# Performance work log

Hardware: AMD Instinct MI355X
Metric: run time of the kernel (lower is better)

Reference implementation:

```python
import jax, jax.numpy as jnp
import numpy as np

S = 2048       # seq_len
D = 1024       # d_model
H = 16         # heads
DK = 64        # d_k = d_v = D // H


def setup_inputs() -> dict:
    key = jax.random.key(0)
    ks = jax.random.split(key, 12)
    sc_in = 1.0 / np.sqrt(D)
    return {
        "Q": jax.random.normal(ks[0], (S, D), jnp.float32),
        "K": jax.random.normal(ks[1], (S, D), jnp.float32),
        "V": jax.random.normal(ks[2], (S, D), jnp.float32),
        # stacked per-head projection weights (torch Linear math: x @ W + b, W stored [in,out])
        "Wq": jax.random.normal(ks[3], (H, D, DK), jnp.float32) * sc_in,
        "bq": jnp.zeros((H, DK), jnp.float32),
        "Wk": jax.random.normal(ks[4], (H, D, DK), jnp.float32) * sc_in,
        "bk": jnp.zeros((H, DK), jnp.float32),
        "Wv": jax.random.normal(ks[5], (H, D, DK), jnp.float32) * sc_in,
        "bv": jnp.zeros((H, DK), jnp.float32),
        "Wo": jax.random.normal(ks[6], (H * DK, D), jnp.float32) * (1.0 / np.sqrt(H * DK)),
        "bo": jnp.zeros((D,), jnp.float32),
    }


def reference(Q, K, V, Wq, bq, Wk, bk, Wv, bv, Wo, bo):
    # per-head projections, all heads at once: [S,D] x [H,D,DK] -> [H,S,DK]
    q = jnp.einsum("sd,hdk->hsk", Q, Wq) + bq[:, None, :]
    k = jnp.einsum("sd,hdk->hsk", K, Wk) + bk[:, None, :]
    v = jnp.einsum("sd,hdk->hsk", V, Wv) + bv[:, None, :]
    # scaled dot-product attention per head: [H,S,S]
    scores = jnp.einsum("hsk,htk->hst", q, k) / jnp.sqrt(jnp.asarray(DK, q.dtype))
    attn = jax.nn.softmax(scores, axis=-1)
    heads = jnp.einsum("hst,htv->hsv", attn, v)          # [H,S,DK]
    concat = heads.transpose(1, 0, 2).reshape(S, H * DK)  # [S, H*DK]
    return concat @ Wo + bo                               # [S, D]
```

## Files before the change

kernel.cpp:

```cpp
#include <hip/hip_runtime.h>
#include <stdint.h>

#define S_LEN 2048
#define D_MODEL 1024
#define NH 16
#define DKV 64

typedef unsigned short u16;
typedef __bf16 bf16x8 __attribute__((ext_vector_type(8)));
typedef float f32x4 __attribute__((ext_vector_type(4)));

__device__ __forceinline__ u16 f2bf(float f) {
  union { float f; uint32_t u; } v; v.f = f;
  uint32_t r = v.u + 0x7FFFu + ((v.u >> 16) & 1u);
  return (u16)(r >> 16);
}
__device__ __forceinline__ uint32_t pkbf(float lo, float hi) {
  union { float f; uint32_t u; } a, b; a.f = lo; b.f = hi;
  return ((b.u + 0x8000u) & 0xFFFF0000u) | ((a.u + 0x8000u) >> 16);
}
__device__ __forceinline__ void gl16(const u16* g, u16* l) {
  __builtin_amdgcn_global_load_lds(
      (const __attribute__((address_space(1))) unsigned int*)g,
      (__attribute__((address_space(3))) unsigned int*)l, 16, 0, 0);
}

__global__ __launch_bounds__(256) void conv_qkv_k(
    const float* __restrict__ Q, const float* __restrict__ K,
    const float* __restrict__ V, u16* __restrict__ out) {
  const float* src = (blockIdx.z == 0) ? Q : (blockIdx.z == 1) ? K : V;
  u16* dst = out + (size_t)blockIdx.z * S_LEN * D_MODEL;
  size_t i = ((size_t)blockIdx.x * blockDim.x + threadIdx.x) * 4;
  const float4 v = *(const float4*)(src + i);
  union { u16 h[4]; uint2 u2; } o;
  o.h[0] = f2bf(v.x); o.h[1] = f2bf(v.y); o.h[2] = f2bf(v.z); o.h[3] = f2bf(v.w);
  *(uint2*)(dst + i) = o.u2;
}

__global__ __launch_bounds__(256) void transpose_qkvw_k(
    const float* __restrict__ Wq, const float* __restrict__ Wk,
    const float* __restrict__ Wv, u16* __restrict__ Wqt,
    u16* __restrict__ Wkt, u16* __restrict__ Wvt) {
  __shared__ float tile[32][33];
  const int which = blockIdx.z >> 4, head = blockIdx.z & 15;
  const float* ip = ((which == 0) ? Wq : (which == 1) ? Wk : Wv) + (size_t)head * D_MODEL * DKV;
  u16* op = ((which == 0) ? Wqt : (which == 1) ? Wkt : Wvt) + (size_t)head * D_MODEL * DKV;
  int r0 = blockIdx.y * 32, c0 = blockIdx.x * 32;
  int tr = threadIdx.x >> 5, tc = threadIdx.x & 31;
#pragma unroll
  for (int i = 0; i < 4; i++)
    tile[tr + i * 8][tc] = ip[(size_t)(r0 + tr + i * 8) * DKV + c0 + tc];
  __syncthreads();
#pragma unroll
  for (int i = 0; i < 4; i++) {
    int c = tr + i * 8;
    op[(size_t)(c0 + c) * D_MODEL + r0 + tc] = f2bf(tile[tc][c]);
  }
}

__global__ __launch_bounds__(256) void transpose_conv_k(
    const float* __restrict__ in, u16* __restrict__ out, int R, int C) {
  __shared__ float tile[32][33];
  int r0 = blockIdx.y * 32, c0 = blockIdx.x * 32;
  int tr = threadIdx.x >> 5, tc = threadIdx.x & 31;
#pragma unroll
  for (int i = 0; i < 4; i++)
    tile[tr + i * 8][tc] = in[(size_t)(r0 + tr + i * 8) * C + c0 + tc];
  __syncthreads();
#pragma unroll
  for (int i = 0; i < 4; i++) {
    int c = tr + i * 8;
    out[(size_t)(c0 + c) * R + r0 + tc] = f2bf(tile[tc][c]);
  }
}

__global__ __launch_bounds__(256, 2) void proj_gemm_k(
    const u16* __restrict__ qkvb, const u16* __restrict__ Wqt,
    const u16* __restrict__ Wkt, const u16* __restrict__ Wvt,
    const float* __restrict__ bq, const float* __restrict__ bk,
    const float* __restrict__ bv,
    u16* __restrict__ qb, u16* __restrict__ kb, u16* __restrict__ vT) {
  const int z = blockIdx.z;
  const int m0 = blockIdx.x * 128, n0 = blockIdx.y * 128;
  const u16* A = qkvb + (size_t)z * S_LEN * D_MODEL;
  const u16* Bt = (z == 0) ? Wqt : (z == 1) ? Wkt : Wvt;
  const float* bias = (z == 0) ? bq : (z == 1) ? bk : bv;
  const float scale = (z == 0) ? 0.18033688f : 1.0f;

  __shared__ __align__(16) u16 smem[4 * 8192];
  const int tid = threadIdx.x;
  const int w = tid >> 6, lane = tid & 63, quad = lane >> 4, l15 = lane & 15;
  const int wm = (w >> 1) * 64, wn = (w & 1) * 64;
  const int pb = w * 256;

  f32x4 acc[4][4] = {};

  {
    u16* As = smem; u16* Bs = smem + 16384;
#pragma unroll
    for (int e = 0; e < 4; e++) {
      int p = pb + e * 64 + lane;
      int r = p >> 3, cg = (p & 7) ^ (r & 7);
      gl16(&A[(size_t)(m0 + r) * D_MODEL + cg * 8], As + (pb + e * 64) * 8);
      gl16(&Bt[(size_t)(n0 + r) * D_MODEL + cg * 8], Bs + (pb + e * 64) * 8);
    }
  }
  for (int it = 0; it < 16; it++) {
    __syncthreads();
    if (it < 15) {
      const int k0 = (it + 1) * 64;
      u16* As = smem + ((it + 1) & 1) * 8192;
      u16* Bs = smem + 16384 + ((it + 1) & 1) * 8192;
#pragma unroll
      for (int e = 0; e < 4; e++) {
        int p = pb + e * 64 + lane;
        int r = p >> 3, cg = (p & 7) ^ (r & 7);
        gl16(&A[(size_t)(m0 + r) * D_MODEL + k0 + cg * 8], As + (pb + e * 64) * 8);
        gl16(&Bt[(size_t)(n0 + r) * D_MODEL + k0 + cg * 8], Bs + (pb + e * 64) * 8);
      }
    }
    const u16* As = smem + (it & 1) * 8192;
    const u16* Bs = smem + 16384 + (it & 1) * 8192;
#pragma unroll
    for (int kc = 0; kc < 2; kc++) {
      bf16x8 af[4], bfr[4];
      const int c = kc * 4 + quad;
#pragma unroll
      for (int t = 0; t < 4; t++) {
        int ma = wm + t * 16 + l15, na = wn + t * 16 + l15;
        af[t] = *(const bf16x8*)&As[(ma * 8 + (c ^ (ma & 7))) * 8];
        bfr[t] = *(const bf16x8*)&Bs[(na * 8 + (c ^ (na & 7))) * 8];
      }
#pragma unroll
      for (int tm = 0; tm < 4; tm++)
#pragma unroll
        for (int tn = 0; tn < 4; tn++)
          acc[tm][tn] = __builtin_amdgcn_mfma_f32_16x16x32_bf16(af[tm], bfr[tn], acc[tm][tn], 0, 0, 0);
    }
  }

  if (z < 2) {
    u16* O = (z == 0) ? qb : kb;
#pragma unroll
    for (int tm = 0; tm < 4; tm++)
#pragma unroll
      for (int tn = 0; tn < 4; tn++)
#pragma unroll
        for (int r = 0; r < 4; r++) {
          int row = m0 + wm + tm * 16 + quad * 4 + r;
          int col = n0 + wn + tn * 16 + l15;
          O[(size_t)row * D_MODEL + col] = f2bf((acc[tm][tn][r] + bias[col]) * scale);
        }
  } else {
#pragma unroll
    for (int tm = 0; tm < 4; tm++)
#pragma unroll
      for (int tn = 0; tn < 4; tn++) {
        int col = n0 + wn + tn * 16 + l15;
        int row0 = m0 + wm + tm * 16 + quad * 4;
        float b = bias[col];
        union { u16 h[4]; uint2 u2; } o;
#pragma unroll
        for (int r = 0; r < 4; r++) o.h[r] = f2bf(acc[tm][tn][r] + b);
        *(uint2*)&vT[(size_t)col * S_LEN + row0] = o.u2;
      }
  }
}

__global__ __launch_bounds__(512) void attn_k(
    const u16* __restrict__ qb, const u16* __restrict__ kb,
    const u16* __restrict__ vT, u16* __restrict__ conc) {
  const int h = blockIdx.y, qblk = blockIdx.x * 64;
  const int tid = threadIdx.x;
  const int w = tid >> 6, lane = tid & 63, quad = lane >> 4, l15 = lane & 15;
  const int half = w >> 2, wq = w & 3;
  const int q0 = qblk + wq * 16;

  __shared__ __align__(16) u16 smem[25600];
  u16* Kh = smem + half * 4096;
  u16* Vh = smem + 8192 + half * 4096;
  u16* Pw = smem + 16384 + w * 1152;

  bf16x8 qf[2];
#pragma unroll
  for (int kc = 0; kc < 2; kc++)
    qf[kc] = *(const bf16x8*)&qb[(size_t)(q0 + l15) * D_MODEL + h * 64 + kc * 32 + quad * 8];

  const int gi = tid & 255;
  const u16* kbase = kb + (size_t)h * 64;
  const u16* vbase = vT + (size_t)(h * 64) * S_LEN;

  f32x4 oacc[4] = {};
  float lsum = 0.f;

  for (int it = 0; it < 16; it++) {
    const int t0 = half * 1024 + it * 64;
#pragma unroll
    for (int j = 0; j < 2; j++) {
      int p = j * 256 + gi;
      int r = p >> 3, cg = (p & 7) ^ (r & 7);
      *(int4*)&Kh[p * 8] = *(const int4*)&kbase[(size_t)(t0 + r) * D_MODEL + cg * 8];
      *(int4*)&Vh[p * 8] = *(const int4*)&vbase[(size_t)r * S_LEN + t0 + cg * 8];
    }
    __syncthreads();

    f32x4 sacc[4] = {};
#pragma unroll
    for (int kc = 0; kc < 2; kc++)
#pragma unroll
      for (int tn = 0; tn < 4; tn++) {
        int rr = tn * 16 + l15;
        bf16x8 ka = *(const bf16x8*)&Kh[(rr * 8 + ((kc * 4 + quad) ^ (l15 & 7))) * 8];
        sacc[tn] = __builtin_amdgcn_mfma_f32_16x16x32_bf16(ka, qf[kc], sacc[tn], 0, 0, 0);
      }

#pragma unroll
    for (int tn = 0; tn < 4; tn++) {
      float p0 = exp2f(sacc[tn][0]);
      float p1 = exp2f(sacc[tn][1]);
      float p2 = exp2f(sacc[tn][2]);
      float p3 = exp2f(sacc[tn][3]);
      lsum += (p0 + p1) + (p2 + p3);
      uint2 pw2; pw2.x = pkbf(p0, p1); pw2.y = pkbf(p2, p3);
      *(uint2*)&Pw[l15 * 72 + tn * 16 + quad * 4] = pw2;
    }

#pragma unroll
    for (int kb2 = 0; kb2 < 2; kb2++) {
      bf16x8 pa = *(const bf16x8*)&Pw[l15 * 72 + kb2 * 32 + quad * 8];
#pragma unroll
      for (int nt = 0; nt < 4; nt++) {
        int rr = nt * 16 + l15;
        bf16x8 vb = *(const bf16x8*)&Vh[(rr * 8 + ((kb2 * 4 + quad) ^ (l15 & 7))) * 8];
        oacc[nt] = __builtin_amdgcn_mfma_f32_16x16x32_bf16(pa, vb, oacc[nt], 0, 0, 0);
      }
    }
    __syncthreads();
  }

  lsum += __shfl_xor(lsum, 16, 64);
  lsum += __shfl_xor(lsum, 32, 64);

  float* OshF = (float*)smem;
  float* lshF = OshF + 8 * 16 * 68;
  if (lane < 16) lshF[w * 16 + lane] = lsum;
#pragma unroll
  for (int nt = 0; nt < 4; nt++)
#pragma unroll
    for (int r = 0; r < 4; r++)
      OshF[w * 1088 + (quad * 4 + r) * 68 + nt * 16 + l15] = oacc[nt][r];
  __syncthreads();

  const int q = tid >> 3;
  const int dv0 = (tid & 7) * 8;
  const int wa = q >> 4, wb = wa + 4, qr = q & 15;
  const float* pa = &OshF[wa * 1088 + qr * 68 + dv0];
  const float* pb = &OshF[wb * 1088 + qr * 68 + dv0];
  float4 a0 = *(const float4*)pa, a1 = *(const float4*)(pa + 4);
  float4 b0 = *(const float4*)pb, b1 = *(const float4*)(pb + 4);
  float li = 1.0f / (lshF[wa * 16 + qr] + lshF[wb * 16 + qr]);
  union { u16 hh[8]; uint4 u4; } o;
  o.hh[0] = f2bf((a0.x + b0.x) * li); o.hh[1] = f2bf((a0.y + b0.y) * li);
  o.hh[2] = f2bf((a0.z + b0.z) * li); o.hh[3] = f2bf((a0.w + b0.w) * li);
  o.hh[4] = f2bf((a1.x + b1.x) * li); o.hh[5] = f2bf((a1.y + b1.y) * li);
  o.hh[6] = f2bf((a1.z + b1.z) * li); o.hh[7] = f2bf((a1.w + b1.w) * li);
  *(uint4*)&conc[(size_t)(qblk + q) * D_MODEL + h * 64 + dv0] = o.u4;
}

__global__ __launch_bounds__(256, 4) void out_gemm_k(
    const u16* __restrict__ A, const u16* __restrict__ Bt,
    const float* __restrict__ bias, float* __restrict__ out) {
  const int n0 = blockIdx.x * 64, m0 = blockIdx.y * 64;
  __shared__ __align__(16) u16 smem[4 * 4096];
  const int tid = threadIdx.x;
  const int w = tid >> 6, lane = tid & 63, quad = lane >> 4, l15 = lane & 15;
  const int wm = (w >> 1) * 32, wn = (w & 1) * 32;
  const int pb = w * 128;

  f32x4 acc[2][2] = {};
  {
    u16* As = smem; u16* Bs = smem + 8192;
#pragma unroll
    for (int e = 0; e < 2; e++) {
      int p = pb + e * 64 + lane;
      int r = p >> 3, cg = (p & 7) ^ (r & 7);
      gl16(&A[(size_t)(m0 + r) * D_MODEL + cg * 8], As + (pb + e * 64) * 8);
      gl16(&Bt[(size_t)(n0 + r) * D_MODEL + cg * 8], Bs + (pb + e * 64) * 8);
    }
  }
  for (int it = 0; it < 16; it++) {
    __syncthreads();
    if (it < 15) {
      const int k0 = (it + 1) * 64;
      u16* As = smem + ((it + 1) & 1) * 4096;
      u16* Bs = smem + 8192 + ((it + 1) & 1) * 4096;
#pragma unroll
      for (int e = 0; e < 2; e++) {
        int p = pb + e * 64 + lane;
        int r = p >> 3, cg = (p & 7) ^ (r & 7);
        gl16(&A[(size_t)(m0 + r) * D_MODEL + k0 + cg * 8], As + (pb + e * 64) * 8);
        gl16(&Bt[(size_t)(n0 + r) * D_MODEL + k0 + cg * 8], Bs + (pb + e * 64) * 8);
      }
    }
    const u16* As = smem + (it & 1) * 4096;
    const u16* Bs = smem + 8192 + (it & 1) * 4096;
#pragma unroll
    for (int kc = 0; kc < 2; kc++) {
      const int c = kc * 4 + quad;
      bf16x8 af[2], bfr[2];
#pragma unroll
      for (int t = 0; t < 2; t++) {
        int ma = wm + t * 16 + l15, na = wn + t * 16 + l15;
        af[t] = *(const bf16x8*)&As[(ma * 8 + (c ^ (ma & 7))) * 8];
        bfr[t] = *(const bf16x8*)&Bs[(na * 8 + (c ^ (na & 7))) * 8];
      }
#pragma unroll
      for (int tm = 0; tm < 2; tm++)
#pragma unroll
        for (int tn = 0; tn < 2; tn++)
          acc[tm][tn] = __builtin_amdgcn_mfma_f32_16x16x32_bf16(af[tm], bfr[tn], acc[tm][tn], 0, 0, 0);
    }
  }
#pragma unroll
  for (int tm = 0; tm < 2; tm++)
#pragma unroll
    for (int tn = 0; tn < 2; tn++)
#pragma unroll
      for (int r = 0; r < 4; r++) {
        int row = m0 + wm + tm * 16 + quad * 4 + r;
        int col = n0 + wn + tn * 16 + l15;
        out[(size_t)row * D_MODEL + col] = acc[tm][tn][r] + bias[col];
      }
}

extern "C" void kernel_launch(void* const* d_in, const int* in_sizes, int n_in,
                              void* d_out, int out_size, void* d_ws, size_t ws_size,
                              hipStream_t stream) {
  const float* Q  = (const float*)d_in[0];
  const float* K  = (const float*)d_in[1];
  const float* V  = (const float*)d_in[2];
  const float* Wq = (const float*)d_in[3];
  const float* bq = (const float*)d_in[4];
  const float* Wk = (const float*)d_in[5];
  const float* bk = (const float*)d_in[6];
  const float* Wv = (const float*)d_in[7];
  const float* bv = (const float*)d_in[8];
  const float* Wo = (const float*)d_in[9];
  const float* bo = (const float*)d_in[10];
  float* out = (float*)d_out;

  u16* ws = (u16*)d_ws;
  u16* QKVb = ws;
  u16* Wqt  = QKVb + (size_t)3 * S_LEN * D_MODEL;
  u16* Wkt  = Wqt + (size_t)D_MODEL * D_MODEL;
  u16* Wvt  = Wkt + (size_t)D_MODEL * D_MODEL;
  u16* Wot  = Wvt + (size_t)D_MODEL * D_MODEL;
  u16* qbuf = Wot + (size_t)D_MODEL * D_MODEL;
  u16* kbuf = qbuf + (size_t)S_LEN * D_MODEL;
  u16* vTb  = kbuf + (size_t)S_LEN * D_MODEL;
  u16* conc = vTb + (size_t)S_LEN * D_MODEL;

  conv_qkv_k<<<dim3(S_LEN * D_MODEL / 1024, 1, 3), 256, 0, stream>>>(Q, K, V, QKVb);
  transpose_qkvw_k<<<dim3(DKV / 32, D_MODEL / 32, NH * 3), 256, 0, stream>>>(
      Wq, Wk, Wv, Wqt, Wkt, Wvt);
  transpose_conv_k<<<dim3(D_MODEL / 32, D_MODEL / 32, 1), 256, 0, stream>>>(Wo, Wot, D_MODEL, D_MODEL);
  proj_gemm_k<<<dim3(S_LEN / 128, D_MODEL / 128, 3), 256, 0, stream>>>(
      QKVb, Wqt, Wkt, Wvt, bq, bk, bv, qbuf, kbuf, vTb);
  attn_k<<<dim3(S_LEN / 64, NH), 512, 0, stream>>>(qbuf, kbuf, vTb, conc);
  out_gemm_k<<<dim3(D_MODEL / 64, S_LEN / 64), 256, 0, stream>>>(conc, Wot, bo, out);
}
```

Before: 175.1 us.

## Double-buffer attention K/V tiles via async LDS loads and merge prep kernels

The attention loop now streams K and V in 32-key tiles into two LDS buffers using global_load_lds. The next tile is prefetched while the current one is being computed, and one of the two barriers per iteration is dropped. The swizzle patterns are adjusted for the new tile shape. Separately, the three preprocessing kernels (input conversion, QKV weight transpose, Wo transpose) are merged into one launch to cut launch overhead. In exchange, the attention loop runs twice as many iterations with fewer MFMAs per barrier.

```diff
diff --git a/kernel.cpp b/kernel.cpp
--- a/kernel.cpp
+++ b/kernel.cpp
@@ -25,52 +25,47 @@
       (__attribute__((address_space(3))) unsigned int*)l, 16, 0, 0);
 }
 
-__global__ __launch_bounds__(256) void conv_qkv_k(
+__global__ __launch_bounds__(256) void prep_k(
     const float* __restrict__ Q, const float* __restrict__ K,
-    const float* __restrict__ V, u16* __restrict__ out) {
-  const float* src = (blockIdx.z == 0) ? Q : (blockIdx.z == 1) ? K : V;
-  u16* dst = out + (size_t)blockIdx.z * S_LEN * D_MODEL;
-  size_t i = ((size_t)blockIdx.x * blockDim.x + threadIdx.x) * 4;
-  const float4 v = *(const float4*)(src + i);
-  union { u16 h[4]; uint2 u2; } o;
-  o.h[0] = f2bf(v.x); o.h[1] = f2bf(v.y); o.h[2] = f2bf(v.z); o.h[3] = f2bf(v.w);
-  *(uint2*)(dst + i) = o.u2;
-}
-
-__global__ __launch_bounds__(256) void transpose_qkvw_k(
-    const float* __restrict__ Wq, const float* __restrict__ Wk,
-    const float* __restrict__ Wv, u16* __restrict__ Wqt,
-    u16* __restrict__ Wkt, u16* __restrict__ Wvt) {
+    const float* __restrict__ V, const float* __restrict__ Wq,
+    const float* __restrict__ Wk, const float* __restrict__ Wv,
+    const float* __restrict__ Wo, u16* __restrict__ QKVb,
+    u16* __restrict__ Wqt, u16* __restrict__ Wkt, u16* __restrict__ Wvt,
+    u16* __restrict__ Wot) {
   __shared__ float tile[32][33];
-  const int which = blockIdx.z >> 4, head = blockIdx.z & 15;
-  const float* ip = ((which == 0) ? Wq : (which == 1) ? Wk : Wv) + (size_t)head * D_MODEL * DKV;
-  u16* op = ((which == 0) ? Wqt : (which == 1) ? Wkt : Wvt) + (size_t)head * D_MODEL * DKV;
-  int r0 = blockIdx.y * 32, c0 = blockIdx.x * 32;
+  const int idx = blockIdx.x;
+  if (idx < 6144) {
+    const int z = idx >> 11, blk = idx & 2047;
+    const float* src = (z == 0) ? Q : (z == 1) ? K : V;
+    u16* dst = QKVb + (size_t)z * S_LEN * D_MODEL;
+    size_t i = ((size_t)blk * 256 + threadIdx.x) * 4;
+    const float4 v = *(const float4*)(src + i);
+    union { u16 h[4]; uint2 u2; } o;
+    o.h[0] = f2bf(v.x); o.h[1] = f2bf(v.y); o.h[2] = f2bf(v.z); o.h[3] = f2bf(v.w);
+    *(uint2*)(dst + i) = o.u2;
+    return;
+  }
+  const float* ip; u16* op; int R, C, r0, c0;
+  if (idx < 9216) {
+    int t = idx - 6144;
+    int which = t >> 10, head = (t & 1023) >> 6, tl = t & 63;
+    ip = ((which == 0) ? Wq : (which == 1) ? Wk : Wv) + (size_t)head * D_MODEL * DKV;
+    op = ((which == 0) ? Wqt : (which == 1) ? Wkt : Wvt) + (size_t)head * D_MODEL * DKV;
+    R = D_MODEL; C = DKV; c0 = (tl & 1) * 32; r0 = (tl >> 1) * 32;
+  } else {
+    int t = idx - 9216;
+    ip = Wo; op = Wot; R = D_MODEL; C = D_MODEL;
+    c0 = (t & 31) * 32; r0 = (t >> 5) * 32;
+  }
   int tr = threadIdx.x >> 5, tc = threadIdx.x & 31;
 #pragma unroll
   for (int i = 0; i < 4; i++)
-    tile[tr + i * 8][tc] = ip[(size_t)(r0 + tr + i * 8) * DKV + c0 + tc];
+    tile[tr + i * 8][tc] = ip[(size_t)(r0 + tr + i * 8) * C + c0 + tc];
   __syncthreads();
 #pragma unroll
   for (int i = 0; i < 4; i++) {
     int c = tr + i * 8;
-    op[(size_t)(c0 + c) * D_MODEL + r0 + tc] = f2bf(tile[tc][c]);
-  }
-}
-
-__global__ __launch_bounds__(256) void transpose_conv_k(
-    const float* __restrict__ in, u16* __restrict__ out, int R, int C) {
-  __shared__ float tile[32][33];
-  int r0 = blockIdx.y * 32, c0 = blockIdx.x * 32;
-  int tr = threadIdx.x >> 5, tc = threadIdx.x & 31;
-#pragma unroll
-  for (int i = 0; i < 4; i++)
-    tile[tr + i * 8][tc] = in[(size_t)(r0 + tr + i * 8) * C + c0 + tc];
-  __syncthreads();
-#pragma unroll
-  for (int i = 0; i < 4; i++) {
-    int c = tr + i * 8;
-    out[(size_t)(c0 + c) * R + r0 + tc] = f2bf(tile[tc][c]);
+    op[(size_t)(c0 + c) * R + r0 + tc] = f2bf(tile[tc][c]);
   }
 }
 
@@ -186,36 +181,49 @@
   for (int kc = 0; kc < 2; kc++)
     qf[kc] = *(const bf16x8*)&qb[(size_t)(q0 + l15) * D_MODEL + h * 64 + kc * 32 + quad * 8];
 
-  const int gi = tid & 255;
   const u16* kbase = kb + (size_t)h * 64;
   const u16* vbase = vT + (size_t)(h * 64) * S_LEN;
 
+  const int p = wq * 64 + lane;
+  const int kr = p >> 3, kcg = (p & 7) ^ (kr & 7);
+  const int vr = p >> 2, vcg = (p & 3) ^ (vr & 3);
+  const size_t kgoff = (size_t)kr * D_MODEL + kcg * 8;
+  const size_t vgoff = (size_t)vr * S_LEN + vcg * 8;
+  const int ldsoff = wq * 64 * 8;
+
   f32x4 oacc[4] = {};
   float lsum = 0.f;
 
-  for (int it = 0; it < 16; it++) {
-    const int t0 = half * 1024 + it * 64;
-#pragma unroll
-    for (int j = 0; j < 2; j++) {
-      int p = j * 256 + gi;
-      int r = p >> 3, cg = (p & 7) ^ (r & 7);
-      *(int4*)&Kh[p * 8] = *(const int4*)&kbase[(size_t)(t0 + r) * D_MODEL + cg * 8];
-      *(int4*)&Vh[p * 8] = *(const int4*)&vbase[(size_t)r * S_LEN + t0 + cg * 8];
-    }
+  {
+    const int t0 = half * 1024;
+    gl16(kbase + (size_t)t0 * D_MODEL + kgoff, Kh + ldsoff);
+    gl16(vbase + t0 + vgoff, Vh + ldsoff);
+  }
+
+  for (int it = 0; it < 32; it++) {
     __syncthreads();
-
-    f32x4 sacc[4] = {};
+    if (it < 31) {
+      const int t0n = half * 1024 + (it + 1) * 32;
+      u16* Kd = Kh + ((it + 1) & 1) * 2048;
+      u16* Vd = Vh + ((it + 1) & 1) * 2048;
+      gl16(kbase + (size_t)t0n * D_MODEL + kgoff, Kd + ldsoff);
+      gl16(vbase + t0n + vgoff, Vd + ldsoff);
+    }
+    const u16* Kc = Kh + (it & 1) * 2048;
+    const u16* Vc = Vh + (it & 1) * 2048;
+
+    f32x4 sacc[2] = {};
 #pragma unroll
     for (int kc = 0; kc < 2; kc++)
 #pragma unroll
-      for (int tn = 0; tn < 4; tn++) {
+      for (int tn = 0; tn < 2; tn++) {
         int rr = tn * 16 + l15;
-        bf16x8 ka = *(const bf16x8*)&Kh[(rr * 8 + ((kc * 4 + quad) ^ (l15 & 7))) * 8];
+        bf16x8 ka = *(const bf16x8*)&Kc[(rr * 8 + ((kc * 4 + quad) ^ (rr & 7))) * 8];
         sacc[tn] = __builtin_amdgcn_mfma_f32_16x16x32_bf16(ka, qf[kc], sacc[tn], 0, 0, 0);
       }
 
 #pragma unroll
-    for (int tn = 0; tn < 4; tn++) {
+    for (int tn = 0; tn < 2; tn++) {
       float p0 = exp2f(sacc[tn][0]);
       float p1 = exp2f(sacc[tn][1]);
       float p2 = exp2f(sacc[tn][2]);
@@ -225,18 +233,15 @@
       *(uint2*)&Pw[l15 * 72 + tn * 16 + quad * 4] = pw2;
     }
 
-#pragma unroll
-    for (int kb2 = 0; kb2 < 2; kb2++) {
-      bf16x8 pa = *(const bf16x8*)&Pw[l15 * 72 + kb2 * 32 + quad * 8];
-#pragma unroll
-      for (int nt = 0; nt < 4; nt++) {
-        int rr = nt * 16 + l15;
-        bf16x8 vb = *(const bf16x8*)&Vh[(rr * 8 + ((kb2 * 4 + quad) ^ (l15 & 7))) * 8];
-        oacc[nt] = __builtin_amdgcn_mfma_f32_16x16x32_bf16(pa, vb, oacc[nt], 0, 0, 0);
-      }
-    }
-    __syncthreads();
-  }
+    bf16x8 pa = *(const bf16x8*)&Pw[l15 * 72 + quad * 8];
+#pragma unroll
+    for (int nt = 0; nt < 4; nt++) {
+      int dv = nt * 16 + l15;
+      bf16x8 vb = *(const bf16x8*)&Vc[(dv * 4 + (quad ^ (dv & 3))) * 8];
+      oacc[nt] = __builtin_amdgcn_mfma_f32_16x16x32_bf16(pa, vb, oacc[nt], 0, 0, 0);
+    }
+  }
+  __syncthreads();
 
   lsum += __shfl_xor(lsum, 16, 64);
   lsum += __shfl_xor(lsum, 32, 64);
@@ -360,10 +365,8 @@
   u16* vTb  = kbuf + (size_t)S_LEN * D_MODEL;
   u16* conc = vTb + (size_t)S_LEN * D_MODEL;
 
-  conv_qkv_k<<<dim3(S_LEN * D_MODEL / 1024, 1, 3), 256, 0, stream>>>(Q, K, V, QKVb);
-  transpose_qkvw_k<<<dim3(DKV / 32, D_MODEL / 32, NH * 3), 256, 0, stream>>>(
-      Wq, Wk, Wv, Wqt, Wkt, Wvt);
-  transpose_conv_k<<<dim3(D_MODEL / 32, D_MODEL / 32, 1), 256, 0, stream>>>(Wo, Wot, D_MODEL, D_MODEL);
+  prep_k<<<dim3(10240), 256, 0, stream>>>(Q, K, V, Wq, Wk, Wv, Wo,
+                                          QKVb, Wqt, Wkt, Wvt, Wot);
   proj_gemm_k<<<dim3(S_LEN / 128, D_MODEL / 128, 3), 256, 0, stream>>>(
       QKVb, Wqt, Wkt, Wvt, bq, bk, bv, qbuf, kbuf, vTb);
   attn_k<<<dim3(S_LEN / 64, NH), 512, 0, stream>>>(qbuf, kbuf, vTb, conc);
```

After: 164.8 us. 5.9% less time.
